# Optimization experiments

Hardware: AMD Instinct MI355X
Metric: run time of the kernel (lower is better)

## Reference

```python
import jax, jax.numpy as jnp
import numpy as np

RES = 256
XYZ_MIN, XYZ_MAX = -1.0, 1.0
STEPSIZE = 1.0
NEAR, FAR, BG = 0.2, 3.0, 1.0
ALPHA_INIT = 0.01
ACT_SHIFT = float(np.log(1.0 / (1.0 - ALPHA_INIT) - 1.0))
VOXEL = (XYZ_MAX - XYZ_MIN) / RES  # (prod(extent)/R^3)^(1/3) = 2/256
N_SAMPLES = int(np.linalg.norm(np.array([RES + 1] * 3, dtype=np.float64)) / STEPSIZE) + 1  # 446
N_RAYS = 4096
LATENT, NFEAT, RGB_LAT = 64, 32, 15
MULTIRES = 6


def _dense(key, din, dout):
    kw, kb = jax.random.split(key)
    return (jax.random.normal(kw, (din, dout), jnp.float32) / np.float32(np.sqrt(din)),
            jax.random.normal(kb, (dout,), jnp.float32) * 0.01)


def setup_inputs():
    ks = jax.random.split(jax.random.key(0), 16)
    rays_o = jax.random.normal(ks[0], (N_RAYS, 3), jnp.float32) * 1.5
    rays_d = jax.random.normal(ks[1], (N_RAYS, 3), jnp.float32)
    viewdirs = rays_d / jnp.linalg.norm(rays_d, axis=-1, keepdims=True)
    mW1, mb1 = _dense(ks[2], 4, 128)
    mW2, mb2 = _dense(ks[3], 128, 128)
    mW3, mb3 = _dense(ks[4], 128, NFEAT)
    pW1, pb1 = _dense(ks[5], LATENT, 64)
    pW2, pb2 = _dense(ks[6], 64, 64)
    pW3, pb3 = _dense(ks[7], 64, 1 + RGB_LAT)
    emb_dim = 3 + 3 * 2 * MULTIRES  # 39
    dW1, db1 = _dense(ks[8], RGB_LAT + emb_dim, 64)
    dW2, db2 = _dense(ks[9], 64, 64)
    dW3, db3 = _dense(ks[10], 64, 64)
    dW4, db4 = _dense(ks[11], 64, 3)
    return dict(
        rays_o=rays_o, rays_d=rays_d, viewdirs=viewdirs,
        mapping_grid=jax.random.normal(ks[12], (4, RES, RES, RES), jnp.float32) * 0.1,
        feature_vectors=jax.random.normal(ks[13], (NFEAT, LATENT), jnp.float32) * 0.1,
        mW1=mW1, mb1=mb1, mW2=mW2, mb2=mb2, mW3=mW3, mb3=mb3,
        pW1=pW1, pb1=pb1, pW2=pW2, pb2=pb2, pW3=pW3, pb3=pb3,
        dW1=dW1, db1=db1, dW2=dW2, db2=db2, dW3=dW3, db3=db3, dW4=dW4, db4=db4)


def _trilinear(grid, pts):
    # grid: [C,R,R,R]; pts: [...,3] world coords; matches F.grid_sample(align_corners=True)
    # after the flip(-1) in the original (x indexes dim0 of the volume).
    g = jnp.transpose(grid, (1, 2, 3, 0))  # [R,R,R,C]
    u = (pts - XYZ_MIN) / (XYZ_MAX - XYZ_MIN)
    idx = jnp.clip(u * (RES - 1), 0.0, RES - 1.0)
    i0 = jnp.clip(jnp.floor(idx).astype(jnp.int32), 0, RES - 2)
    f = idx - i0.astype(idx.dtype)
    x0, y0, z0 = i0[..., 0], i0[..., 1], i0[..., 2]
    x1, y1, z1 = x0 + 1, y0 + 1, z0 + 1
    fx, fy, fz = f[..., 0:1], f[..., 1:2], f[..., 2:3]
    c000, c001 = g[x0, y0, z0], g[x0, y0, z1]
    c010, c011 = g[x0, y1, z0], g[x0, y1, z1]
    c100, c101 = g[x1, y0, z0], g[x1, y0, z1]
    c110, c111 = g[x1, y1, z0], g[x1, y1, z1]
    c00 = c000 * (1 - fz) + c001 * fz
    c01 = c010 * (1 - fz) + c011 * fz
    c10 = c100 * (1 - fz) + c101 * fz
    c11 = c110 * (1 - fz) + c111 * fz
    c0 = c00 * (1 - fy) + c01 * fy
    c1 = c10 * (1 - fy) + c11 * fy
    return c0 * (1 - fx) + c1 * fx


def _mlp3(x, W1, b1, W2, b2, W3, b3):
    h = jax.nn.relu(x @ W1 + b1)
    h = jax.nn.relu(h @ W2 + b2)
    return h @ W3 + b3


def _dir_embed(v):
    # NeRF positional encoding: [v, sin(2^i v), cos(2^i v)] for i in [0, MULTIRES)
    freqs = 2.0 ** jnp.arange(MULTIRES, dtype=v.dtype)  # [L]
    ang = v[..., None, :] * freqs[:, None]              # [N,L,3]
    sc = jnp.concatenate([jnp.sin(ang), jnp.cos(ang)], axis=-1)  # [N,L,6]
    return jnp.concatenate([v, sc.reshape(v.shape[0], 2 * 3 * MULTIRES)], axis=-1)  # [N,39]


def reference(rays_o, rays_d, viewdirs, mapping_grid, feature_vectors,
              mW1, mb1, mW2, mb2, mW3, mb3,
              pW1, pb1, pW2, pb2, pW3, pb3,
              dW1, db1, dW2, db2, dW3, db3, dW4, db4):
    # --- ray sampling (is_train=False, no jitter) ---
    vec = jnp.where(rays_d == 0, 1e-6, rays_d)
    rate_a = (XYZ_MAX - rays_o) / vec
    rate_b = (XYZ_MIN - rays_o) / vec
    t_min = jnp.clip(jnp.minimum(rate_a, rate_b).max(-1), NEAR, FAR)
    t_max = jnp.clip(jnp.maximum(rate_a, rate_b).min(-1), NEAR, FAR)
    step = STEPSIZE * VOXEL * jnp.arange(N_SAMPLES, dtype=rays_o.dtype)  # [S]
    interpx = t_min[:, None] + step[None, :] / jnp.linalg.norm(rays_d, axis=-1, keepdims=True)
    ray_pts = rays_o[:, None, :] + rays_d[:, None, :] * interpx[..., None]  # [N,S,3]
    valid = ~((t_max <= t_min)[:, None]
              | jnp.any((ray_pts < XYZ_MIN) | (ray_pts > XYZ_MAX), axis=-1))  # [N,S]

    # --- latent extraction: grid sample -> attention over feature bank ---
    mp = _trilinear(mapping_grid, ray_pts)                                  # [N,S,4]
    attn = jax.nn.softmax(_mlp3(mp, mW1, mb1, mW2, mb2, mW3, mb3), axis=-1)  # [N,S,F]
    latent = attn @ feature_vectors                                          # [N,S,latent]

    # --- positional MLP -> density + rgb latent (masked entries zeroed as in torch) ---
    pos = _mlp3(latent, pW1, pb1, pW2, pb2, pW3, pb3)  # [N,S,1+rgb_lat]
    alpha = jnp.where(valid,
                      1.0 - jnp.exp(-jax.nn.softplus(pos[..., 0] + ACT_SHIFT) * STEPSIZE),
                      0.0)
    rgb_latent = jnp.where(valid[..., None], pos[..., 1:], 0.0)

    # --- alpha compositing weights ---
    alphainv_cum = jnp.concatenate(
        [jnp.ones_like(alpha[..., :1]),
         jnp.cumprod(jnp.clip(1.0 - alpha, 1e-10, None), axis=-1)], axis=-1)  # [N,S+1]
    weights = alpha * alphainv_cum[..., :-1]

    # --- directional MLP -> rgb ---
    emb = _dir_embed(viewdirs)                                               # [N,39]
    emb = jnp.broadcast_to(emb[:, None, :], (alpha.shape[0], alpha.shape[1], emb.shape[-1]))
    rgb_feat = jnp.concatenate([rgb_latent, emb], axis=-1)                   # [N,S,54]
    h = jax.nn.relu(rgb_feat @ dW1 + db1)
    h = jax.nn.relu(h @ dW2 + db2)
    h = jax.nn.relu(h @ dW3 + db3)
    raw_rgb = h @ dW4 + db4
    rgb = jnp.where(valid[..., None], jax.nn.sigmoid(raw_rgb[..., :3]), 0.0)

    rgb_marched = jnp.einsum('ns,nsc->nc', weights, rgb) + alphainv_cum[..., -1:] * BG
    return rgb_marched
```

## Files before the change

kernel.cpp:

```cpp
#include <hip/hip_runtime.h>
#include <math.h>

#define ACT_SHIFT -4.5951198501345889f
#define SB 128
#define NSLOTMAX (4096*446)
#define MLP_BLOCKS 768

typedef _Float16 f16;
typedef f16 f16x8 __attribute__((ext_vector_type(8)));
typedef f16 f16x4 __attribute__((ext_vector_type(4)));
typedef f16 f16x2 __attribute__((ext_vector_type(2)));
typedef float f32x4 __attribute__((ext_vector_type(4)));
typedef float f32x16 __attribute__((ext_vector_type(16)));

#define OFF_CNT  0
#define OFF_RAYI 256
#define OFF_RAYF (OFF_RAYI + 4096*16)
#define OFF_EMBW (OFF_RAYF + 4096*8)
#define OFF_WTS  (OFF_EMBW + 4096*64*4)
#define OFF_BIAS (OFF_WTS + 92160)
#define OFF_SLOT (OFF_BIAS + 8192)
#define OFF_WS4H (OFF_SLOT + NSLOTMAX*4)

#define W_MW1 0
#define W_MW2 2048
#define W_MW3 18432
#define W_FV  22528
#define W_P1  24576
#define W_P2  28672
#define W_P3  32768
#define W_D1  34816
#define W_D2  35840
#define W_D3  39936
#define W_D4  44032
#define W_TOT 46080

static __device__ __forceinline__ unsigned short f2h(float x) {
  f16 h = (f16)x; return *(unsigned short*)&h;
}
static __device__ __forceinline__ float h2f(unsigned short u) {
  return (float)(*(f16*)&u);
}

static __device__ __forceinline__ void bar_lds() {
  asm volatile("s_waitcnt lgkmcnt(0)" ::: "memory");
  __builtin_amdgcn_s_barrier();
}

static __device__ __forceinline__ void sample_point(
    float ox, float oy, float oz, float dx, float dy, float dz,
    float tmin, float nrm, int s, float& px, float& py, float& pz) {
  float ix = tmin + (0.0078125f * (float)s) / nrm;
  px = ox + dx * ix; py = oy + dy * ix; pz = oz + dz * ix;
}
static __device__ __forceinline__ int in_box(float px, float py, float pz) {
  return !(px < -1.f || px > 1.f || py < -1.f || py > 1.f ||
           pz < -1.f || pz > 1.f);
}

static __device__ __forceinline__ bool ray_setup(
    const float* rays_o, const float* rays_d, int r,
    float& ox, float& oy, float& oz, float& dx, float& dy, float& dz,
    float& tmin, float& nrm) {
  ox = rays_o[r*3+0]; oy = rays_o[r*3+1]; oz = rays_o[r*3+2];
  dx = rays_d[r*3+0]; dy = rays_d[r*3+1]; dz = rays_d[r*3+2];
  const float vx = (dx == 0.0f) ? 1e-6f : dx;
  const float vy = (dy == 0.0f) ? 1e-6f : dy;
  const float vz = (dz == 0.0f) ? 1e-6f : dz;
  const float rax = ( 1.0f - ox) / vx, rbx = (-1.0f - ox) / vx;
  const float ray_ = ( 1.0f - oy) / vy, rby = (-1.0f - oy) / vy;
  const float raz = ( 1.0f - oz) / vz, rbz = (-1.0f - oz) / vz;
  tmin = fmaxf(fmaxf(fminf(rax,rbx), fminf(ray_,rby)), fminf(raz,rbz));
  tmin = fminf(fmaxf(tmin, 0.2f), 3.0f);
  float tmax = fminf(fminf(fmaxf(rax,rbx), fmaxf(ray_,rby)), fmaxf(raz,rbz));
  tmax = fminf(fmaxf(tmax, 0.2f), 3.0f);
  nrm = sqrtf(dx*dx + dy*dy + dz*dz);
  return tmax <= tmin;
}

extern "C" __global__ void __launch_bounds__(256)
k_setup(const float* __restrict__ rays_o, const float* __restrict__ rays_d,
        int* __restrict__ cnt, int4* __restrict__ rayi,
        float2* __restrict__ rayf) {
  int r = blockIdx.x * 256 + threadIdx.x;
  if (r >= 4096) return;
  float ox,oy,oz,dx,dy,dz,tmin,nrm;
  bool miss = ray_setup(rays_o, rays_d, r, ox,oy,oz,dx,dy,dz, tmin, nrm);
  rayf[r] = make_float2(tmin, nrm);
  if (miss) { rayi[r] = make_int4(0,0,0,0); return; }

  float lo = -1e30f, hi = 1e30f;
  float o3[3] = {ox,oy,oz}, d3[3] = {dx,dy,dz};
#pragma unroll
  for (int c = 0; c < 3; ++c) {
    float o = o3[c], d = d3[c];
    if (d == 0.0f) {
      if (o < -1.f || o > 1.f) { lo = 1e30f; hi = -1e30f; }
    } else {
      float t1 = (-1.f - o) / d, t2 = (1.f - o) / d;
      lo = fmaxf(lo, fminf(t1, t2));
      hi = fminf(hi, fmaxf(t1, t2));
    }
  }
  float k = 0.0078125f / nrm;
  float sf = (lo - tmin) / k - 1.0f;
  float lf = (hi - tmin) / k + 1.0f;
  int first = (int)ceilf (fmaxf(0.f,  fminf(445.f, sf)));
  int last  = (int)floorf(fmaxf(-1.f, fminf(445.f, lf)));
  int n_s = (lf >= sf && last >= first) ? (last - first + 1) : 0;
  int base = 0;
  if (n_s > 0) base = atomicAdd(cnt, n_s);
  rayi[r] = make_int4(base, first, n_s, 0);
}

extern "C" __global__ void __launch_bounds__(256)
k_aux(const float* __restrict__ viewdirs, const int4* __restrict__ rayi,
      int* __restrict__ slot_map,
      const float* __restrict__ mW1, const float* __restrict__ mW2,
      const float* __restrict__ mW3, const float* __restrict__ fv,
      const float* __restrict__ pW1, const float* __restrict__ pW2,
      const float* __restrict__ pW3, const float* __restrict__ dW1,
      const float* __restrict__ dW2, const float* __restrict__ dW3,
      const float* __restrict__ dW4,
      const float* __restrict__ mb1, const float* __restrict__ mb2,
      const float* __restrict__ mb3, const float* __restrict__ pb1,
      const float* __restrict__ pb2, const float* __restrict__ pb3,
      const float* __restrict__ db1, const float* __restrict__ db2,
      const float* __restrict__ db3, const float* __restrict__ db4,
      f16* __restrict__ wts, float* __restrict__ bias,
      float* __restrict__ embW) {
  const int b = blockIdx.x, t = threadIdx.x;
  if (b < 1024) {
    int idx = b * 256 + t;
    int ray = idx >> 6, o = idx & 63;
    float v0 = viewdirs[ray*3+0], v1 = viewdirs[ray*3+1], v2 = viewdirs[ray*3+2];
    float acc = db1[o];
    acc = fmaf(v0, dW1[15*64+o], acc);
    acc = fmaf(v1, dW1[16*64+o], acc);
    acc = fmaf(v2, dW1[17*64+o], acc);
#pragma unroll
    for (int fr = 0; fr < 6; ++fr) {
      float f = (float)(1 << fr);
      int rb = 18 + fr*6;
      acc = fmaf(sinf(v0*f), dW1[(rb+0)*64+o], acc);
      acc = fmaf(sinf(v1*f), dW1[(rb+1)*64+o], acc);
      acc = fmaf(sinf(v2*f), dW1[(rb+2)*64+o], acc);
      acc = fmaf(cosf(v0*f), dW1[(rb+3)*64+o], acc);
      acc = fmaf(cosf(v1*f), dW1[(rb+4)*64+o], acc);
      acc = fmaf(cosf(v2*f), dW1[(rb+5)*64+o], acc);
    }
    embW[idx] = acc;
  } else if (b < 1280) {
    int ray = (b - 1024) * 16 + (t >> 4);
    int4 ri = rayi[ray];
    for (int i = t & 15; i < ri.z; i += 16)
      slot_map[ri.x + i] = (ray << 9) | (ri.y + i);
  } else if (b < 1460) {
    int i = (b - 1280) * 256 + t;
    if (i >= W_TOT) return;
    float v = 0.f; int l, o, k;
    if (i < W_MW2)      { l=i;        o=l>>4; k=l&15;  if (k<4)  v = mW1[k*128+o]; }
    else if (i < W_MW3) { l=i-W_MW2;  o=l>>7; k=l&127; v = mW2[k*128+o]; }
    else if (i < W_FV)  { l=i-W_MW3;  o=l>>7; k=l&127; v = mW3[k*32+o]; }
    else if (i < W_P1)  { l=i-W_FV;   o=l>>5; k=l&31;  v = fv[k*64+o]; }
    else if (i < W_P2)  { l=i-W_P1;   o=l>>6; k=l&63;  v = pW1[k*64+o]; }
    else if (i < W_P3)  { l=i-W_P2;   o=l>>6; k=l&63;  v = pW2[k*64+o]; }
    else if (i < W_D1)  { l=i-W_P3;   o=l>>6; k=l&63;  if (o<16) v = pW3[k*16+o]; }
    else if (i < W_D2)  { l=i-W_D1;   o=l>>4; k=l&15;  if (k>=1) v = dW1[(k-1)*64+o]; }
    else if (i < W_D3)  { l=i-W_D2;   o=l>>6; k=l&63;  v = dW2[k*64+o]; }
    else if (i < W_D4)  { l=i-W_D3;   o=l>>6; k=l&63;  v = dW3[k*64+o]; }
    else                { l=i-W_D4;   o=l>>6; k=l&63;  if (o<3)  v = dW4[k*3+o]; }
    wts[i] = (f16)v;
  } else {
    int i = (b - 1460) * 256 + t;
    if (i >= 1408) return;
    int L = i >> 7, o = i & 127;
    float v = 0.f;
    if      (L == 0)            v = mb1[o];
    else if (L == 1)            v = mb2[o];
    else if (L == 2 && o < 32)  v = mb3[o];
    else if (L == 4 && o < 64)  v = pb1[o];
    else if (L == 5 && o < 64)  v = pb2[o];
    else if (L == 6 && o < 16)  v = pb3[o];
    else if (L == 8 && o < 64)  v = db2[o];
    else if (L == 9 && o < 64)  v = db3[o];
    else if (L == 10 && o < 3)  v = db4[o];
    bias[i] = v;
  }
}

template<int KS>
static __device__ __forceinline__ void load_b(const f16* Xb, int st, int lane,
                                              f16x8* B) {
  const int r = st*32 + (lane & 31);
  const int base = r*256 + ((lane >> 5) * 16);
#pragma unroll
  for (int ks = 0; ks < KS; ++ks) {
    int off = (base + ks*32) ^ ((r & 15) << 4);
    B[ks] = *(const f16x8*)((const char*)Xb + off);
  }
}

template<int KS>
static __device__ __forceinline__ void load_a(const f16* __restrict__ wbase,
                                              int dt, int lane, f16x8* A) {
  const f16* wp = wbase + (size_t)(dt*32 + (lane & 31)) * (KS*16) + (lane >> 5) * 8;
#pragma unroll
  for (int ks = 0; ks < KS; ++ks) A[ks] = *(const f16x8*)(wp + ks*16);
}

template<int KS>
static __device__ __forceinline__ f32x16 mm(const f16x8* A, const f16x8* B) {
  f32x16 acc;
#pragma unroll
  for (int i = 0; i < 16; ++i) acc[i] = 0.f;
#pragma unroll
  for (int ks = 0; ks < KS; ++ks)
    acc = __builtin_amdgcn_mfma_f32_32x32x16_f16(A[ks], B[ks], acc, 0, 0, 0);
  return acc;
}

template<bool RELU, int NQ>
static __device__ __forceinline__ void store_c(f16* Yb, int st, int dtb, int lane,
                                               const f32x16& acc,
                                               const float* __restrict__ bp) {
  const int r = st*32 + (lane & 31);
  const int gp = (lane >> 5) * 4;
#pragma unroll
  for (int q = 0; q < NQ; ++q) {
    const int db = dtb + q*8 + gp;
    f32x4 b4 = *(const f32x4*)(bp + db);
    float v0 = acc[4*q+0]+b4[0], v1 = acc[4*q+1]+b4[1];
    float v2 = acc[4*q+2]+b4[2], v3 = acc[4*q+3]+b4[3];
    if (RELU) {
      v0 = fmaxf(v0,0.f); v1 = fmaxf(v1,0.f);
      v2 = fmaxf(v2,0.f); v3 = fmaxf(v3,0.f);
    }
    f16x4 o = {(f16)v0,(f16)v1,(f16)v2,(f16)v3};
    int off = (r*256 + db*2) ^ ((r & 15) << 4);
    *(f16x4*)((char*)Yb + off) = o;
  }
}

struct Pf {
  float v[8];
  float fx, fy, fz;
  int pk;
};

static __device__ __forceinline__ void pf_issue(
    int slot, int total, int c,
    const int* __restrict__ slot_map, const float2* __restrict__ rayf,
    const float* __restrict__ rays_o, const float* __restrict__ rays_d,
    const float* __restrict__ grid, Pf& P) {
  if (slot >= total) {
    P.pk = -2; P.fx = P.fy = P.fz = 0.f;
#pragma unroll
    for (int i = 0; i < 8; ++i) P.v[i] = 0.f;
    return;
  }
  int mi = slot_map[slot];
  int ray = mi >> 9, s = mi & 511;
  float2 tf = rayf[ray];
  float ox = rays_o[ray*3+0], oy = rays_o[ray*3+1], oz = rays_o[ray*3+2];
  float dx = rays_d[ray*3+0], dy = rays_d[ray*3+1], dz = rays_d[ray*3+2];
  float px, py, pz;
  sample_point(ox,oy,oz,dx,dy,dz, tf.x, tf.y, s, px,py,pz);
  P.pk = ray*2 + in_box(px,py,pz);
  float ixf = fminf(fmaxf((px + 1.f) * 0.5f * 255.f, 0.f), 255.f);
  float iyf = fminf(fmaxf((py + 1.f) * 0.5f * 255.f, 0.f), 255.f);
  float izf = fminf(fmaxf((pz + 1.f) * 0.5f * 255.f, 0.f), 255.f);
  int x0 = min((int)ixf, 254), y0 = min((int)iyf, 254), z0 = min((int)izf, 254);
  P.fx = ixf - (float)x0; P.fy = iyf - (float)y0; P.fz = izf - (float)z0;
  const float* gc = grid + (size_t)c * 16777216u;
  int bx0 = x0 << 16, bx1 = bx0 + 65536;
  int by0 = y0 << 8,  by1 = by0 + 256;
  P.v[0] = gc[bx0+by0+z0]; P.v[1] = gc[bx0+by0+z0+1];
  P.v[2] = gc[bx0+by1+z0]; P.v[3] = gc[bx0+by1+z0+1];
  P.v[4] = gc[bx1+by0+z0]; P.v[5] = gc[bx1+by0+z0+1];
  P.v[6] = gc[bx1+by1+z0]; P.v[7] = gc[bx1+by1+z0+1];
}

extern "C" __global__ void __launch_bounds__(512, 4)
k_mlp(const float* __restrict__ rays_o, const float* __restrict__ rays_d,
      const float* __restrict__ grid, const int* __restrict__ slot_map,
      const float2* __restrict__ rayf, const float* __restrict__ embW,
      const f16* __restrict__ wts, const float* __restrict__ bias,
      int* __restrict__ cnt, unsigned short* __restrict__ ws4h) {
  const int total = cnt[0];
  const int nch = (total + 127) >> 7;
  int* qh = cnt + 1;
  const int tid = threadIdx.x;
  const int wv = tid >> 6, lane = tid & 63;
  const int sl = tid >> 2, ch = tid & 3;
  const int dthi = wv >> 2;
  const int stw = wv & 3;

  __shared__ __align__(16) f16 X[SB*128];
  __shared__ __align__(16) f16 Y[SB*128];
  __shared__ int sinfo[SB];
  __shared__ int q_next;

  if (tid == 0) q_next = atomicAdd(qh, 1);
  __syncthreads();
  int cur = q_next;

  Pf P;
  pf_issue((cur < nch) ? cur*128 + sl : total, total, ch,
           slot_map, rayf, rays_o, rays_d, grid, P);

  while (cur < nch) {
    const int blockbase = cur << 7;
    if (tid == 0) q_next = atomicAdd(qh, 1);

    {
      float c00 = P.v[0]*(1.f-P.fz) + P.v[1]*P.fz;
      float c01 = P.v[2]*(1.f-P.fz) + P.v[3]*P.fz;
      float c10 = P.v[4]*(1.f-P.fz) + P.v[5]*P.fz;
      float c11 = P.v[6]*(1.f-P.fz) + P.v[7]*P.fz;
      float c0v = c00*(1.f-P.fy) + c01*P.fy;
      float c1v = c10*(1.f-P.fy) + c11*P.fy;
      float mv  = c0v*(1.f-P.fx) + c1v*P.fx;
      if (ch == 0) sinfo[sl] = P.pk;
      int off = (sl*256 + ch*2) ^ ((sl & 15) << 4);
      *(f16*)((char*)X + off) = (f16)mv;
      if (ch < 3) {
        int zo = (sl*256 + 8 + ch*8) ^ ((sl & 15) << 4);
        *(unsigned long long*)((char*)X + zo) = 0ull;
      }
    }
    bar_lds();
    const int nxt = q_next;
    pf_issue((nxt < nch) ? nxt*128 + sl : total, total, ch,
             slot_map, rayf, rays_o, rays_d, grid, P);

    float alpha_reg = 0.f; int pk_reg = -2;

    { f16x8 B[1]; load_b<1>(X, stw, lane, B);
      f16x8 A1[1];
      load_a<1>(wts+W_MW1, dthi, lane, A1);
      f32x16 a0 = mm<1>(A1, B);
      store_c<true,4>(Y, stw, dthi*32, lane, a0, bias + 0*128);
      load_a<1>(wts+W_MW1, dthi+2, lane, A1);
      f32x16 a1 = mm<1>(A1, B);
      store_c<true,4>(Y, stw, (dthi+2)*32, lane, a1, bias + 0*128);
    } bar_lds();

    { f16x8 B[8]; load_b<8>(Y, stw, lane, B);
      f16x8 A8[8];
      load_a<8>(wts+W_MW2, dthi, lane, A8);
      f32x16 a0 = mm<8>(A8, B);
      store_c<true,4>(X, stw, dthi*32, lane, a0, bias + 1*128);
      load_a<8>(wts+W_MW2, dthi+2, lane, A8);
      f32x16 a1 = mm<8>(A8, B);
      store_c<true,4>(X, stw, (dthi+2)*32, lane, a1, bias + 1*128);
    } bar_lds();

    if (wv < 4) {
      f16x8 B[8]; load_b<8>(X, wv, lane, B);
      f16x8 A8[8]; load_a<8>(wts+W_MW3, 0, lane, A8);
      f32x16 acc = mm<8>(A8, B);
      const int gp = (lane >> 5) * 4;
      float v[16];
#pragma unroll
      for (int q = 0; q < 4; ++q) {
        f32x4 b4 = *(const f32x4*)(bias + 2*128 + q*8 + gp);
#pragma unroll
        for (int i = 0; i < 4; ++i) v[4*q+i] = acc[4*q+i] + b4[i];
      }
      float mx = v[0];
#pragma unroll
      for (int i = 1; i < 16; ++i) mx = fmaxf(mx, v[i]);
      mx = fmaxf(mx, __shfl_xor(mx, 32));
      float s = 0.f;
#pragma unroll
      for (int i = 0; i < 16; ++i) { v[i] = expf(v[i] - mx); s += v[i]; }
      s += __shfl_xor(s, 32);
      float inv = 1.f / s;
      const int r = wv*32 + (lane & 31);
#pragma unroll
      for (int q = 0; q < 4; ++q) {
        const int db = q*8 + gp;
        f16x4 o = {(f16)(v[4*q+0]*inv), (f16)(v[4*q+1]*inv),
                   (f16)(v[4*q+2]*inv), (f16)(v[4*q+3]*inv)};
        int off = (r*256 + db*2) ^ ((r & 15) << 4);
        *(f16x4*)((char*)Y + off) = o;
      }
    }
    bar_lds();

    { f16x8 B[2]; load_b<2>(Y, stw, lane, B);
      f16x8 A2[2]; load_a<2>(wts+W_FV, dthi, lane, A2);
      f32x16 a0 = mm<2>(A2, B);
      store_c<false,4>(X, stw, dthi*32, lane, a0, bias + 3*128);
    } bar_lds();

    { f16x8 B[4]; load_b<4>(X, stw, lane, B);
      f16x8 A4[4]; load_a<4>(wts+W_P1, dthi, lane, A4);
      f32x16 a0 = mm<4>(A4, B);
      store_c<true,4>(Y, stw, dthi*32, lane, a0, bias + 4*128);
    } bar_lds();

    { f16x8 B[4]; load_b<4>(Y, stw, lane, B);
      f16x8 A4[4]; load_a<4>(wts+W_P2, dthi, lane, A4);
      f32x16 a0 = mm<4>(A4, B);
      store_c<true,4>(X, stw, dthi*32, lane, a0, bias + 5*128);
    } bar_lds();

    if (wv < 4) {
      f16x8 B[4]; load_b<4>(X, wv, lane, B);
      f16x8 A4[4]; load_a<4>(wts+W_P3, 0, lane, A4);
      f32x16 acc = mm<4>(A4, B);
      pk_reg = sinfo[wv*32 + (lane & 31)];
      if (lane < 32) {
        alpha_reg = 0.f;
        if (pk_reg >= 0 && (pk_reg & 1)) {
          float x = acc[0] + bias[6*128 + 0] + ACT_SHIFT;
          float sp = fmaxf(x, 0.f) + log1pf(expf(-fabsf(x)));
          alpha_reg = 1.f - expf(-sp);
        }
      }
      store_c<false,2>(Y, wv, 0, lane, acc, bias + 6*128);
    }
    bar_lds();

    { f16x8 B[1]; load_b<1>(Y, stw, lane, B);
      f16x8 A1[1]; load_a<1>(wts+W_D1, dthi, lane, A1);
      f32x16 acc = mm<1>(A1, B);
      int pkc = sinfo[stw*32 + (lane & 31)];
      int ry = (pkc < 0) ? 0 : (pkc >> 1);
      store_c<true,4>(X, stw, dthi*32, lane, acc, embW + (size_t)ry*64);
    } bar_lds();

    { f16x8 B[4]; load_b<4>(X, stw, lane, B);
      f16x8 A4[4]; load_a<4>(wts+W_D2, dthi, lane, A4);
      f32x16 a0 = mm<4>(A4, B);
      store_c<true,4>(Y, stw, dthi*32, lane, a0, bias + 8*128);
    } bar_lds();

    { f16x8 B[4]; load_b<4>(Y, stw, lane, B);
      f16x8 A4[4]; load_a<4>(wts+W_D3, dthi, lane, A4);
      f32x16 a0 = mm<4>(A4, B);
      store_c<true,4>(X, stw, dthi*32, lane, a0, bias + 9*128);
    } bar_lds();

    if (wv < 4) {
      f16x8 B[4]; load_b<4>(X, wv, lane, B);
      f16x8 A4[4]; load_a<4>(wts+W_D4, 0, lane, A4);
      f32x16 acc = mm<4>(A4, B);
      if (lane < 32 && pk_reg >= 0) {
        const float* bp = bias + 10*128;
        bool val = (pk_reg & 1) != 0;
        ushort4 u;
        u.x = f2h(alpha_reg);
        u.y = f2h(val ? 1.f/(1.f+expf(-(acc[0]+bp[0]))) : 0.f);
        u.z = f2h(val ? 1.f/(1.f+expf(-(acc[1]+bp[1]))) : 0.f);
        u.w = f2h(val ? 1.f/(1.f+expf(-(acc[2]+bp[2]))) : 0.f);
        *(ushort4*)(ws4h + (size_t)(blockbase + wv*32 + (lane & 31))*4) = u;
      }
    }
    bar_lds();
    cur = nxt;
  }
}

extern "C" __global__ void __launch_bounds__(256)
k_scan(const ushort4* __restrict__ ws4h, const int4* __restrict__ rayi,
       float* __restrict__ out) {
  const int wid = (blockIdx.x * 256 + threadIdx.x) >> 6;
  const int ln  = threadIdx.x & 63;
  if (wid >= 4096) return;
  int4 ri = rayi[wid];
  int base = ri.x, n_s = ri.z;

  float T = 1.0f, ar = 0.f, ag = 0.f, ab = 0.f;
  int nc = (n_s + 63) >> 6;
  for (int cck = 0; cck < nc; ++cck) {
    int j = cck*64 + ln;
    float a = 0.f, rr = 0.f, gg = 0.f, bb = 0.f;
    if (j < n_s) {
      ushort4 u = ws4h[(size_t)base + j];
      a = h2f(u.x); rr = h2f(u.y); gg = h2f(u.z); bb = h2f(u.w);
    }
    float p = fmaxf(1.0f - a, 1e-10f);
#pragma unroll
    for (int off = 1; off < 64; off <<= 1) {
      float o = __shfl_up(p, off);
      if (ln >= off) p *= o;
    }
    float pe = __shfl_up(p, 1);
    if (ln == 0) pe = 1.0f;
    float wgt = a * T * pe;
    ar = fmaf(wgt, rr, ar);
    ag = fmaf(wgt, gg, ag);
    ab = fmaf(wgt, bb, ab);
    T *= __shfl(p, 63);
  }
#pragma unroll
  for (int off = 32; off; off >>= 1) {
    ar += __shfl_down(ar, off);
    ag += __shfl_down(ag, off);
    ab += __shfl_down(ab, off);
  }
  if (ln == 0) {
    out[wid*3+0] = ar + T;
    out[wid*3+1] = ag + T;
    out[wid*3+2] = ab + T;
  }
}

extern "C" void kernel_launch(void* const* d_in, const int* in_sizes, int n_in,
                              void* d_out, int out_size, void* d_ws, size_t ws_size,
                              hipStream_t stream) {
  const float* rays_o   = (const float*)d_in[0];
  const float* rays_d   = (const float*)d_in[1];
  const float* viewdirs = (const float*)d_in[2];
  const float* grid     = (const float*)d_in[3];
  const float* fv       = (const float*)d_in[4];
  const float* mW1 = (const float*)d_in[5];  const float* mb1 = (const float*)d_in[6];
  const float* mW2 = (const float*)d_in[7];  const float* mb2 = (const float*)d_in[8];
  const float* mW3 = (const float*)d_in[9];  const float* mb3 = (const float*)d_in[10];
  const float* pW1 = (const float*)d_in[11]; const float* pb1 = (const float*)d_in[12];
  const float* pW2 = (const float*)d_in[13]; const float* pb2 = (const float*)d_in[14];
  const float* pW3 = (const float*)d_in[15]; const float* pb3 = (const float*)d_in[16];
  const float* dW1 = (const float*)d_in[17]; const float* db1 = (const float*)d_in[18];
  const float* dW2 = (const float*)d_in[19]; const float* db2 = (const float*)d_in[20];
  const float* dW3 = (const float*)d_in[21]; const float* db3 = (const float*)d_in[22];
  const float* dW4 = (const float*)d_in[23]; const float* db4 = (const float*)d_in[24];
  float* out = (float*)d_out;

  char* ws = (char*)d_ws;
  int*     cnt      = (int*)(ws + OFF_CNT);
  int4*    rayi     = (int4*)(ws + OFF_RAYI);
  float2*  rayf     = (float2*)(ws + OFF_RAYF);
  float*   embW     = (float*)(ws + OFF_EMBW);
  f16*     wts      = (f16*)(ws + OFF_WTS);
  float*   bias     = (float*)(ws + OFF_BIAS);
  int*     slot_map = (int*)(ws + OFF_SLOT);
  unsigned short* ws4h = (unsigned short*)(ws + OFF_WS4H);

  hipMemsetAsync(cnt, 0, 8, stream);
  k_setup<<<16, 256, 0, stream>>>(rays_o, rays_d, cnt, rayi, rayf);
  k_aux<<<1466, 256, 0, stream>>>(viewdirs, rayi, slot_map,
                                  mW1, mW2, mW3, fv, pW1, pW2, pW3,
                                  dW1, dW2, dW3, dW4,
                                  mb1, mb2, mb3, pb1, pb2, pb3,
                                  db1, db2, db3, db4, wts, bias, embW);
  k_mlp<<<MLP_BLOCKS, 512, 0, stream>>>(rays_o, rays_d, grid, slot_map, rayf,
                                        embW, wts, bias, cnt, ws4h);
  k_scan<<<1024, 256, 0, stream>>>((const ushort4*)ws4h, rayi, out);
}
```

Baseline: 125.9 us.

## Keep MLP activations in registers per wave, dropping LDS staging and barriers

The MLP kernel is restructured so that each wave independently processes 32 samples through every layer. Activations stay in registers and are converted from MFMA output layout to B-operand layout with a cross-half shuffle, replacing the LDS round trips and block-wide barriers between layers. The atomic work queue and the software prefetch of grid samples are replaced by a static grid-stride loop, and the block shape becomes 1024 blocks of 256 threads. The cost is high register pressure from holding the P/Q operand arrays, and there is no longer any overlap of gather latency with compute.

```diff
diff --git a/kernel.cpp b/kernel.cpp
--- a/kernel.cpp
+++ b/kernel.cpp
@@ -2,15 +2,10 @@
 #include <math.h>
 
 #define ACT_SHIFT -4.5951198501345889f
-#define SB 128
 #define NSLOTMAX (4096*446)
-#define MLP_BLOCKS 768
 
 typedef _Float16 f16;
 typedef f16 f16x8 __attribute__((ext_vector_type(8)));
-typedef f16 f16x4 __attribute__((ext_vector_type(4)));
-typedef f16 f16x2 __attribute__((ext_vector_type(2)));
-typedef float f32x4 __attribute__((ext_vector_type(4)));
 typedef float f32x16 __attribute__((ext_vector_type(16)));
 
 #define OFF_CNT  0
@@ -41,10 +36,17 @@
 static __device__ __forceinline__ float h2f(unsigned short u) {
   return (float)(*(f16*)&u);
 }
-
-static __device__ __forceinline__ void bar_lds() {
-  asm volatile("s_waitcnt lgkmcnt(0)" ::: "memory");
-  __builtin_amdgcn_s_barrier();
+static __device__ __forceinline__ unsigned pack2(float a, float b) {
+  f16 ha = (f16)a, hb = (f16)b;
+  unsigned short ua, ub;
+  __builtin_memcpy(&ua, &ha, 2); __builtin_memcpy(&ub, &hb, 2);
+  return (unsigned)ua | ((unsigned)ub << 16);
+}
+static __device__ __forceinline__ f16x8 mkb(unsigned w0, unsigned w1,
+                                            unsigned w2, unsigned w3) {
+  union { unsigned u[4]; f16x8 h; } x;
+  x.u[0] = w0; x.u[1] = w1; x.u[2] = w2; x.u[3] = w3;
+  return x.h;
 }
 
 static __device__ __forceinline__ void sample_point(
@@ -190,277 +192,236 @@
 }
 
 template<int KS>
-static __device__ __forceinline__ void load_b(const f16* Xb, int st, int lane,
-                                              f16x8* B) {
-  const int r = st*32 + (lane & 31);
-  const int base = r*256 + ((lane >> 5) * 16);
-#pragma unroll
-  for (int ks = 0; ks < KS; ++ks) {
-    int off = (base + ks*32) ^ ((r & 15) << 4);
-    B[ks] = *(const f16x8*)((const char*)Xb + off);
-  }
-}
-
-template<int KS>
-static __device__ __forceinline__ void load_a(const f16* __restrict__ wbase,
-                                              int dt, int lane, f16x8* A) {
+static __device__ __forceinline__ f32x16 tile_mm(const f16* __restrict__ wbase,
+                                                 int dt, int lane,
+                                                 const f16x8* B) {
   const f16* wp = wbase + (size_t)(dt*32 + (lane & 31)) * (KS*16) + (lane >> 5) * 8;
-#pragma unroll
-  for (int ks = 0; ks < KS; ++ks) A[ks] = *(const f16x8*)(wp + ks*16);
-}
-
-template<int KS>
-static __device__ __forceinline__ f32x16 mm(const f16x8* A, const f16x8* B) {
   f32x16 acc;
 #pragma unroll
   for (int i = 0; i < 16; ++i) acc[i] = 0.f;
 #pragma unroll
   for (int ks = 0; ks < KS; ++ks)
-    acc = __builtin_amdgcn_mfma_f32_32x32x16_f16(A[ks], B[ks], acc, 0, 0, 0);
+    acc = __builtin_amdgcn_mfma_f32_32x32x16_f16(*(const f16x8*)(wp + ks*16),
+                                                 B[ks], acc, 0, 0, 0);
   return acc;
 }
 
-template<bool RELU, int NQ>
-static __device__ __forceinline__ void store_c(f16* Yb, int st, int dtb, int lane,
-                                               const f32x16& acc,
-                                               const float* __restrict__ bp) {
-  const int r = st*32 + (lane & 31);
-  const int gp = (lane >> 5) * 4;
-#pragma unroll
-  for (int q = 0; q < NQ; ++q) {
-    const int db = dtb + q*8 + gp;
-    f32x4 b4 = *(const f32x4*)(bp + db);
-    float v0 = acc[4*q+0]+b4[0], v1 = acc[4*q+1]+b4[1];
-    float v2 = acc[4*q+2]+b4[2], v3 = acc[4*q+3]+b4[3];
-    if (RELU) {
-      v0 = fmaxf(v0,0.f); v1 = fmaxf(v1,0.f);
-      v2 = fmaxf(v2,0.f); v3 = fmaxf(v3,0.f);
-    }
-    f16x4 o = {(f16)v0,(f16)v1,(f16)v2,(f16)v3};
-    int off = (r*256 + db*2) ^ ((r & 15) << 4);
-    *(f16x4*)((char*)Yb + off) = o;
-  }
-}
-
-struct Pf {
-  float v[8];
-  float fx, fy, fz;
-  int pk;
-};
-
-static __device__ __forceinline__ void pf_issue(
-    int slot, int total, int c,
-    const int* __restrict__ slot_map, const float2* __restrict__ rayf,
-    const float* __restrict__ rays_o, const float* __restrict__ rays_d,
-    const float* __restrict__ grid, Pf& P) {
-  if (slot >= total) {
-    P.pk = -2; P.fx = P.fy = P.fz = 0.f;
-#pragma unroll
-    for (int i = 0; i < 8; ++i) P.v[i] = 0.f;
-    return;
-  }
-  int mi = slot_map[slot];
-  int ray = mi >> 9, s = mi & 511;
-  float2 tf = rayf[ray];
-  float ox = rays_o[ray*3+0], oy = rays_o[ray*3+1], oz = rays_o[ray*3+2];
-  float dx = rays_d[ray*3+0], dy = rays_d[ray*3+1], dz = rays_d[ray*3+2];
-  float px, py, pz;
-  sample_point(ox,oy,oz,dx,dy,dz, tf.x, tf.y, s, px,py,pz);
-  P.pk = ray*2 + in_box(px,py,pz);
-  float ixf = fminf(fmaxf((px + 1.f) * 0.5f * 255.f, 0.f), 255.f);
-  float iyf = fminf(fmaxf((py + 1.f) * 0.5f * 255.f, 0.f), 255.f);
-  float izf = fminf(fmaxf((pz + 1.f) * 0.5f * 255.f, 0.f), 255.f);
-  int x0 = min((int)ixf, 254), y0 = min((int)iyf, 254), z0 = min((int)izf, 254);
-  P.fx = ixf - (float)x0; P.fy = iyf - (float)y0; P.fz = izf - (float)z0;
-  const float* gc = grid + (size_t)c * 16777216u;
-  int bx0 = x0 << 16, bx1 = bx0 + 65536;
-  int by0 = y0 << 8,  by1 = by0 + 256;
-  P.v[0] = gc[bx0+by0+z0]; P.v[1] = gc[bx0+by0+z0+1];
-  P.v[2] = gc[bx0+by1+z0]; P.v[3] = gc[bx0+by1+z0+1];
-  P.v[4] = gc[bx1+by0+z0]; P.v[5] = gc[bx1+by0+z0+1];
-  P.v[6] = gc[bx1+by1+z0]; P.v[7] = gc[bx1+by1+z0+1];
-}
-
-extern "C" __global__ void __launch_bounds__(512, 4)
+static __device__ __forceinline__ void h_to_b(const float* h, int g,
+                                              f16x8& b0, f16x8& b1) {
+#pragma unroll
+  for (int kk = 0; kk < 2; ++kk) {
+    unsigned pA0 = pack2(h[8*kk+0], h[8*kk+1]);
+    unsigned pA1 = pack2(h[8*kk+2], h[8*kk+3]);
+    unsigned pB0 = pack2(h[8*kk+4], h[8*kk+5]);
+    unsigned pB1 = pack2(h[8*kk+6], h[8*kk+7]);
+    unsigned s0 = g ? pA0 : pB0;
+    unsigned s1 = g ? pA1 : pB1;
+    unsigned r0 = (unsigned)__shfl_xor((int)s0, 32);
+    unsigned r1 = (unsigned)__shfl_xor((int)s1, 32);
+    unsigned k0 = g ? pB0 : pA0;
+    unsigned k1 = g ? pB1 : pA1;
+    f16x8 b = mkb(g ? r0 : k0, g ? r1 : k1, g ? k0 : r0, g ? k1 : r1);
+    if (kk == 0) b0 = b; else b1 = b;
+  }
+}
+
+#define DOUTI(r) (((r)&3) + 8*((r)>>2) + 4*g)
+
+extern "C" __global__ void __launch_bounds__(256, 4)
 k_mlp(const float* __restrict__ rays_o, const float* __restrict__ rays_d,
       const float* __restrict__ grid, const int* __restrict__ slot_map,
       const float2* __restrict__ rayf, const float* __restrict__ embW,
       const f16* __restrict__ wts, const float* __restrict__ bias,
-      int* __restrict__ cnt, unsigned short* __restrict__ ws4h) {
+      const int* __restrict__ cnt, unsigned short* __restrict__ ws4h) {
   const int total = cnt[0];
-  const int nch = (total + 127) >> 7;
-  int* qh = cnt + 1;
+  const int ngrp = (total + 31) >> 5;
   const int tid = threadIdx.x;
   const int wv = tid >> 6, lane = tid & 63;
-  const int sl = tid >> 2, ch = tid & 3;
-  const int dthi = wv >> 2;
-  const int stw = wv & 3;
-
-  __shared__ __align__(16) f16 X[SB*128];
-  __shared__ __align__(16) f16 Y[SB*128];
-  __shared__ int sinfo[SB];
-  __shared__ int q_next;
-
-  if (tid == 0) q_next = atomicAdd(qh, 1);
-  __syncthreads();
-  int cur = q_next;
-
-  Pf P;
-  pf_issue((cur < nch) ? cur*128 + sl : total, total, ch,
-           slot_map, rayf, rays_o, rays_d, grid, P);
-
-  while (cur < nch) {
-    const int blockbase = cur << 7;
-    if (tid == 0) q_next = atomicAdd(qh, 1);
+  const int g = lane >> 5, col = lane & 31;
+  const int stride = gridDim.x * 4;
+
+  for (int grp = blockIdx.x*4 + wv; grp < ngrp; grp += stride) {
+    const int slot = grp*32 + col;
+
+    int pk = -2;
+    float m0 = 0.f, m1 = 0.f;
+    if (slot < total) {
+      int mi = slot_map[slot];
+      int ray = mi >> 9, s = mi & 511;
+      float2 tf = rayf[ray];
+      float ox = rays_o[ray*3+0], oy = rays_o[ray*3+1], oz = rays_o[ray*3+2];
+      float dx = rays_d[ray*3+0], dy = rays_d[ray*3+1], dz = rays_d[ray*3+2];
+      float px, py, pz;
+      sample_point(ox,oy,oz,dx,dy,dz, tf.x, tf.y, s, px,py,pz);
+      pk = ray*2 + in_box(px,py,pz);
+      float ixf = fminf(fmaxf((px + 1.f) * 0.5f * 255.f, 0.f), 255.f);
+      float iyf = fminf(fmaxf((py + 1.f) * 0.5f * 255.f, 0.f), 255.f);
+      float izf = fminf(fmaxf((pz + 1.f) * 0.5f * 255.f, 0.f), 255.f);
+      int x0 = min((int)ixf, 254), y0 = min((int)iyf, 254), z0 = min((int)izf, 254);
+      float fx = ixf - (float)x0, fy = iyf - (float)y0, fz = izf - (float)z0;
+      int bx0 = x0 << 16, bx1 = bx0 + 65536;
+      int by0 = y0 << 8,  by1 = by0 + 256;
+#pragma unroll
+      for (int q = 0; q < 2; ++q) {
+        const float* gc = grid + (size_t)(2*g + q) * 16777216u;
+        float c000 = gc[bx0+by0+z0], c001 = gc[bx0+by0+z0+1];
+        float c010 = gc[bx0+by1+z0], c011 = gc[bx0+by1+z0+1];
+        float c100 = gc[bx1+by0+z0], c101 = gc[bx1+by0+z0+1];
+        float c110 = gc[bx1+by1+z0], c111 = gc[bx1+by1+z0+1];
+        float c00 = c000*(1.f-fz) + c001*fz;
+        float c01 = c010*(1.f-fz) + c011*fz;
+        float c10 = c100*(1.f-fz) + c101*fz;
+        float c11 = c110*(1.f-fz) + c111*fz;
+        float c0v = c00*(1.f-fy) + c01*fy;
+        float c1v = c10*(1.f-fy) + c11*fy;
+        float mv = c0v*(1.f-fx) + c1v*fx;
+        if (q == 0) m0 = mv; else m1 = mv;
+      }
+    }
+    const int ry = (pk < 0) ? 0 : (pk >> 1);
+    float alpha = 0.f;
+
+    unsigned xw = pack2(m0, m1);
+    unsigned yw = (unsigned)__shfl_xor((int)xw, 32);
+    f16x8 bI = mkb(g ? 0u : xw, g ? 0u : yw, 0u, 0u);
+
+    f16x8 P[8], Q[8];
+
+#pragma unroll
+    for (int dt = 0; dt < 4; ++dt) {
+      f32x16 a = tile_mm<1>(wts + W_MW1, dt, lane, &bI);
+      float h[16];
+#pragma unroll
+      for (int r = 0; r < 16; ++r)
+        h[r] = fmaxf(a[r] + bias[0*128 + dt*32 + DOUTI(r)], 0.f);
+      h_to_b(h, g, P[2*dt], P[2*dt+1]);
+    }
+    __builtin_amdgcn_sched_barrier(0);
+
+#pragma unroll
+    for (int dt = 0; dt < 4; ++dt) {
+      f32x16 a = tile_mm<8>(wts + W_MW2, dt, lane, P);
+      float h[16];
+#pragma unroll
+      for (int r = 0; r < 16; ++r)
+        h[r] = fmaxf(a[r] + bias[1*128 + dt*32 + DOUTI(r)], 0.f);
+      h_to_b(h, g, Q[2*dt], Q[2*dt+1]);
+    }
+    __builtin_amdgcn_sched_barrier(0);
 
     {
-      float c00 = P.v[0]*(1.f-P.fz) + P.v[1]*P.fz;
-      float c01 = P.v[2]*(1.f-P.fz) + P.v[3]*P.fz;
-      float c10 = P.v[4]*(1.f-P.fz) + P.v[5]*P.fz;
-      float c11 = P.v[6]*(1.f-P.fz) + P.v[7]*P.fz;
-      float c0v = c00*(1.f-P.fy) + c01*P.fy;
-      float c1v = c10*(1.f-P.fy) + c11*P.fy;
-      float mv  = c0v*(1.f-P.fx) + c1v*P.fx;
-      if (ch == 0) sinfo[sl] = P.pk;
-      int off = (sl*256 + ch*2) ^ ((sl & 15) << 4);
-      *(f16*)((char*)X + off) = (f16)mv;
-      if (ch < 3) {
-        int zo = (sl*256 + 8 + ch*8) ^ ((sl & 15) << 4);
-        *(unsigned long long*)((char*)X + zo) = 0ull;
-      }
-    }
-    bar_lds();
-    const int nxt = q_next;
-    pf_issue((nxt < nch) ? nxt*128 + sl : total, total, ch,
-             slot_map, rayf, rays_o, rays_d, grid, P);
-
-    float alpha_reg = 0.f; int pk_reg = -2;
-
-    { f16x8 B[1]; load_b<1>(X, stw, lane, B);
-      f16x8 A1[1];
-      load_a<1>(wts+W_MW1, dthi, lane, A1);
-      f32x16 a0 = mm<1>(A1, B);
-      store_c<true,4>(Y, stw, dthi*32, lane, a0, bias + 0*128);
-      load_a<1>(wts+W_MW1, dthi+2, lane, A1);
-      f32x16 a1 = mm<1>(A1, B);
-      store_c<true,4>(Y, stw, (dthi+2)*32, lane, a1, bias + 0*128);
-    } bar_lds();
-
-    { f16x8 B[8]; load_b<8>(Y, stw, lane, B);
-      f16x8 A8[8];
-      load_a<8>(wts+W_MW2, dthi, lane, A8);
-      f32x16 a0 = mm<8>(A8, B);
-      store_c<true,4>(X, stw, dthi*32, lane, a0, bias + 1*128);
-      load_a<8>(wts+W_MW2, dthi+2, lane, A8);
-      f32x16 a1 = mm<8>(A8, B);
-      store_c<true,4>(X, stw, (dthi+2)*32, lane, a1, bias + 1*128);
-    } bar_lds();
-
-    if (wv < 4) {
-      f16x8 B[8]; load_b<8>(X, wv, lane, B);
-      f16x8 A8[8]; load_a<8>(wts+W_MW3, 0, lane, A8);
-      f32x16 acc = mm<8>(A8, B);
-      const int gp = (lane >> 5) * 4;
+      f32x16 a = tile_mm<8>(wts + W_MW3, 0, lane, Q);
       float v[16];
 #pragma unroll
-      for (int q = 0; q < 4; ++q) {
-        f32x4 b4 = *(const f32x4*)(bias + 2*128 + q*8 + gp);
-#pragma unroll
-        for (int i = 0; i < 4; ++i) v[4*q+i] = acc[4*q+i] + b4[i];
-      }
+      for (int r = 0; r < 16; ++r)
+        v[r] = a[r] + bias[2*128 + DOUTI(r)];
       float mx = v[0];
 #pragma unroll
-      for (int i = 1; i < 16; ++i) mx = fmaxf(mx, v[i]);
+      for (int r = 1; r < 16; ++r) mx = fmaxf(mx, v[r]);
       mx = fmaxf(mx, __shfl_xor(mx, 32));
       float s = 0.f;
 #pragma unroll
-      for (int i = 0; i < 16; ++i) { v[i] = expf(v[i] - mx); s += v[i]; }
+      for (int r = 0; r < 16; ++r) { v[r] = expf(v[r] - mx); s += v[r]; }
       s += __shfl_xor(s, 32);
       float inv = 1.f / s;
-      const int r = wv*32 + (lane & 31);
-#pragma unroll
-      for (int q = 0; q < 4; ++q) {
-        const int db = q*8 + gp;
-        f16x4 o = {(f16)(v[4*q+0]*inv), (f16)(v[4*q+1]*inv),
-                   (f16)(v[4*q+2]*inv), (f16)(v[4*q+3]*inv)};
-        int off = (r*256 + db*2) ^ ((r & 15) << 4);
-        *(f16x4*)((char*)Y + off) = o;
+#pragma unroll
+      for (int r = 0; r < 16; ++r) v[r] *= inv;
+      h_to_b(v, g, P[0], P[1]);
+    }
+    __builtin_amdgcn_sched_barrier(0);
+
+#pragma unroll
+    for (int dt = 0; dt < 2; ++dt) {
+      f32x16 a = tile_mm<2>(wts + W_FV, dt, lane, P);
+      float h[16];
+#pragma unroll
+      for (int r = 0; r < 16; ++r) h[r] = a[r];
+      h_to_b(h, g, Q[2*dt], Q[2*dt+1]);
+    }
+    __builtin_amdgcn_sched_barrier(0);
+
+#pragma unroll
+    for (int dt = 0; dt < 2; ++dt) {
+      f32x16 a = tile_mm<4>(wts + W_P1, dt, lane, Q);
+      float h[16];
+#pragma unroll
+      for (int r = 0; r < 16; ++r)
+        h[r] = fmaxf(a[r] + bias[4*128 + dt*32 + DOUTI(r)], 0.f);
+      h_to_b(h, g, P[2*dt], P[2*dt+1]);
+    }
+    __builtin_amdgcn_sched_barrier(0);
+
+#pragma unroll
+    for (int dt = 0; dt < 2; ++dt) {
+      f32x16 a = tile_mm<4>(wts + W_P2, dt, lane, P);
+      float h[16];
+#pragma unroll
+      for (int r = 0; r < 16; ++r)
+        h[r] = fmaxf(a[r] + bias[5*128 + dt*32 + DOUTI(r)], 0.f);
+      h_to_b(h, g, Q[2*dt], Q[2*dt+1]);
+    }
+    __builtin_amdgcn_sched_barrier(0);
+
+    {
+      f32x16 a = tile_mm<4>(wts + W_P3, 0, lane, Q);
+      float h[16];
+#pragma unroll
+      for (int r = 0; r < 16; ++r)
+        h[r] = a[r] + bias[6*128 + DOUTI(r)];
+      if (pk >= 0 && (pk & 1)) {
+        float x = h[0] + ACT_SHIFT;
+        float sp = fmaxf(x, 0.f) + log1pf(expf(-fabsf(x)));
+        alpha = 1.f - expf(-sp);
       }
-    }
-    bar_lds();
-
-    { f16x8 B[2]; load_b<2>(Y, stw, lane, B);
-      f16x8 A2[2]; load_a<2>(wts+W_FV, dthi, lane, A2);
-      f32x16 a0 = mm<2>(A2, B);
-      store_c<false,4>(X, stw, dthi*32, lane, a0, bias + 3*128);
-    } bar_lds();
-
-    { f16x8 B[4]; load_b<4>(X, stw, lane, B);
-      f16x8 A4[4]; load_a<4>(wts+W_P1, dthi, lane, A4);
-      f32x16 a0 = mm<4>(A4, B);
-      store_c<true,4>(Y, stw, dthi*32, lane, a0, bias + 4*128);
-    } bar_lds();
-
-    { f16x8 B[4]; load_b<4>(Y, stw, lane, B);
-      f16x8 A4[4]; load_a<4>(wts+W_P2, dthi, lane, A4);
-      f32x16 a0 = mm<4>(A4, B);
-      store_c<true,4>(X, stw, dthi*32, lane, a0, bias + 5*128);
-    } bar_lds();
-
-    if (wv < 4) {
-      f16x8 B[4]; load_b<4>(X, wv, lane, B);
-      f16x8 A4[4]; load_a<4>(wts+W_P3, 0, lane, A4);
-      f32x16 acc = mm<4>(A4, B);
-      pk_reg = sinfo[wv*32 + (lane & 31)];
-      if (lane < 32) {
-        alpha_reg = 0.f;
-        if (pk_reg >= 0 && (pk_reg & 1)) {
-          float x = acc[0] + bias[6*128 + 0] + ACT_SHIFT;
-          float sp = fmaxf(x, 0.f) + log1pf(expf(-fabsf(x)));
-          alpha_reg = 1.f - expf(-sp);
-        }
+      h_to_b(h, g, P[0], P[1]);
+    }
+    __builtin_amdgcn_sched_barrier(0);
+
+#pragma unroll
+    for (int dt = 0; dt < 2; ++dt) {
+      f32x16 a = tile_mm<1>(wts + W_D1, dt, lane, P);
+      float h[16];
+#pragma unroll
+      for (int r = 0; r < 16; ++r)
+        h[r] = fmaxf(a[r] + embW[(size_t)ry*64 + dt*32 + DOUTI(r)], 0.f);
+      h_to_b(h, g, Q[2*dt], Q[2*dt+1]);
+    }
+    __builtin_amdgcn_sched_barrier(0);
+
+#pragma unroll
+    for (int dt = 0; dt < 2; ++dt) {
+      f32x16 a = tile_mm<4>(wts + W_D2, dt, lane, Q);
+      float h[16];
+#pragma unroll
+      for (int r = 0; r < 16; ++r)
+        h[r] = fmaxf(a[r] + bias[8*128 + dt*32 + DOUTI(r)], 0.f);
+      h_to_b(h, g, P[2*dt], P[2*dt+1]);
+    }
+    __builtin_amdgcn_sched_barrier(0);
+
+#pragma unroll
+    for (int dt = 0; dt < 2; ++dt) {
+      f32x16 a = tile_mm<4>(wts + W_D3, dt, lane, P);
+      float h[16];
+#pragma unroll
+      for (int r = 0; r < 16; ++r)
+        h[r] = fmaxf(a[r] + bias[9*128 + dt*32 + DOUTI(r)], 0.f);
+      h_to_b(h, g, Q[2*dt], Q[2*dt+1]);
+    }
+    __builtin_amdgcn_sched_barrier(0);
+
+    {
+      f32x16 a = tile_mm<4>(wts + W_D4, 0, lane, Q);
+      if (g == 0 && pk >= 0) {
+        bool val = (pk & 1) != 0;
+        ushort4 u;
+        u.x = f2h(alpha);
+        u.y = f2h(val ? 1.f/(1.f+expf(-(a[0] + bias[10*128+0]))) : 0.f);
+        u.z = f2h(val ? 1.f/(1.f+expf(-(a[1] + bias[10*128+1]))) : 0.f);
+        u.w = f2h(val ? 1.f/(1.f+expf(-(a[2] + bias[10*128+2]))) : 0.f);
+        *(ushort4*)(ws4h + (size_t)slot*4) = u;
       }
-      store_c<false,2>(Y, wv, 0, lane, acc, bias + 6*128);
-    }
-    bar_lds();
-
-    { f16x8 B[1]; load_b<1>(Y, stw, lane, B);
-      f16x8 A1[1]; load_a<1>(wts+W_D1, dthi, lane, A1);
-      f32x16 acc = mm<1>(A1, B);
-      int pkc = sinfo[stw*32 + (lane & 31)];
-      int ry = (pkc < 0) ? 0 : (pkc >> 1);
-      store_c<true,4>(X, stw, dthi*32, lane, acc, embW + (size_t)ry*64);
-    } bar_lds();
-
-    { f16x8 B[4]; load_b<4>(X, stw, lane, B);
-      f16x8 A4[4]; load_a<4>(wts+W_D2, dthi, lane, A4);
-      f32x16 a0 = mm<4>(A4, B);
-      store_c<true,4>(Y, stw, dthi*32, lane, a0, bias + 8*128);
-    } bar_lds();
-
-    { f16x8 B[4]; load_b<4>(Y, stw, lane, B);
-      f16x8 A4[4]; load_a<4>(wts+W_D3, dthi, lane, A4);
-      f32x16 a0 = mm<4>(A4, B);
-      store_c<true,4>(X, stw, dthi*32, lane, a0, bias + 9*128);
-    } bar_lds();
-
-    if (wv < 4) {
-      f16x8 B[4]; load_b<4>(X, wv, lane, B);
-      f16x8 A4[4]; load_a<4>(wts+W_D4, 0, lane, A4);
-      f32x16 acc = mm<4>(A4, B);
-      if (lane < 32 && pk_reg >= 0) {
-        const float* bp = bias + 10*128;
-        bool val = (pk_reg & 1) != 0;
-        ushort4 u;
-        u.x = f2h(alpha_reg);
-        u.y = f2h(val ? 1.f/(1.f+expf(-(acc[0]+bp[0]))) : 0.f);
-        u.z = f2h(val ? 1.f/(1.f+expf(-(acc[1]+bp[1]))) : 0.f);
-        u.w = f2h(val ? 1.f/(1.f+expf(-(acc[2]+bp[2]))) : 0.f);
-        *(ushort4*)(ws4h + (size_t)(blockbase + wv*32 + (lane & 31))*4) = u;
-      }
-    }
-    bar_lds();
-    cur = nxt;
+    }
   }
 }
 
@@ -546,7 +507,7 @@
                                   dW1, dW2, dW3, dW4,
                                   mb1, mb2, mb3, pb1, pb2, pb3,
                                   db1, db2, db3, db4, wts, bias, embW);
-  k_mlp<<<MLP_BLOCKS, 512, 0, stream>>>(rays_o, rays_d, grid, slot_map, rayf,
-                                        embW, wts, bias, cnt, ws4h);
+  k_mlp<<<1024, 256, 0, stream>>>(rays_o, rays_d, grid, slot_map, rayf,
+                                  embW, wts, bias, cnt, ws4h);
   k_scan<<<1024, 256, 0, stream>>>((const ushort4*)ws4h, rayi, out);
 }
```

Result: slower. 351.0 us (+178.7%).
